# Kernel tuning notes

Measured on AMD Instinct MI355X. Metric: run time of the kernel, lower is better.

## Reference

```python
import jax, jax.numpy as jnp
import numpy as np

B, S, DM, H, HD = 2, 2048, 1024, 16, 64
MEM_SIZE = 1000
K_SIMILAR, K_CONTIG = 8, 2
K_TOTAL = K_SIMILAR + K_CONTIG  # 10 memory tokens
NEG = -1e9


def setup_inputs() -> dict:
    key = jax.random.key(0)
    k1, k2, k3, k4, k5, k6 = jax.random.split(key, 6)
    inputs = jax.random.normal(k1, (B, S, DM), dtype=jnp.float32)
    attention_mask = jnp.ones((B, S), dtype=jnp.float32)
    Wq = jax.random.normal(k2, (DM, H * HD), dtype=jnp.float32) * 0.02
    Wk = jax.random.normal(k3, (DM, H * HD), dtype=jnp.float32) * 0.02
    Wv = jax.random.normal(k4, (DM, H * HD), dtype=jnp.float32) * 0.02
    Wo = jax.random.normal(k5, (H * HD, DM), dtype=jnp.float32) * 0.02
    events = jax.random.normal(k6, (MEM_SIZE, H * HD), dtype=jnp.float32) * 0.02
    return {"inputs": inputs, "attention_mask": attention_mask,
            "Wq": Wq, "Wk": Wk, "Wv": Wv, "Wo": Wo, "events": events}


def _forward(inputs, attention_mask, Wq, Wk, Wv, Wo, events):
    # projections (no bias), split heads: [B, H, S, HD]
    q = (inputs @ Wq).reshape(B, S, H, HD).transpose(0, 2, 1, 3)
    k = (inputs @ Wk).reshape(B, S, H, HD).transpose(0, 2, 1, 3)
    v = (inputs @ Wv).reshape(B, S, H, HD).transpose(0, 2, 1, 3)

    # --- episodic retrieval: cosine top-k of last-token key vs events ---
    qvec = k[:, :, -1, :].reshape(B, H * HD)                       # [B, D]
    qn = qvec / (jnp.linalg.norm(qvec, axis=-1, keepdims=True) + 1e-8)
    en = events / (jnp.linalg.norm(events, axis=-1, keepdims=True) + 1e-8)
    sims = qn @ en.T                                               # [B, M]
    _, topk_idx = jax.lax.top_k(sims, K_TOTAL)                     # [B, K]
    retrieved = events[topk_idx]                                   # [B, K, D]
    retrieved_k = retrieved.reshape(B, K_TOTAL, H, HD).transpose(0, 2, 1, 3)  # [B,H,K,HD]
    retrieved_v = retrieved_k                                      # non-differential path

    aug_k = jnp.concatenate([retrieved_k, k], axis=2)              # [B,H,K+S,HD]
    aug_v = jnp.concatenate([retrieved_v, v], axis=2)

    # --- ALiBi bias: slopes * (pos_i - pos_j) on original cols, 0 on memory cols ---
    slopes = 2.0 ** (-8.0 * jnp.arange(1, H + 1, dtype=jnp.float32) / H)  # [H]
    positions = jnp.arange(S, dtype=jnp.float32)
    pos_diff = positions[:, None] - positions[None, :]             # [S, S]
    alibi = slopes[:, None, None] * pos_diff                       # [H, S, S]
    alibi = jnp.concatenate([jnp.zeros((H, S, K_TOTAL), jnp.float32), alibi], axis=-1)

    # --- causal mask: -1e9 strictly-upper on original cols, 0 on memory cols ---
    tri = jnp.where(jnp.arange(S)[None, :] > jnp.arange(S)[:, None], NEG, 0.0)  # [S,S]
    causal = jnp.concatenate([jnp.zeros((S, K_TOTAL), jnp.float32), tri], axis=-1)

    # --- padding mask: memory tokens always attendable ---
    aug_mask = jnp.concatenate([jnp.ones((B, K_TOTAL), jnp.float32), attention_mask], axis=-1)
    mask_bias = (1.0 - aug_mask)[:, None, None, :] * NEG           # [B,1,1,K+S]

    scores = jnp.einsum("bhqd,bhkd->bhqk", q, aug_k) / np.sqrt(HD)
    scores = scores + alibi[None] + causal[None, None] + mask_bias
    attn = jax.nn.softmax(scores, axis=-1)
    out = jnp.einsum("bhqk,bhkd->bhqd", attn, aug_v)               # [B,H,S,HD]
    out = out.transpose(0, 2, 1, 3).reshape(B, S, H * HD)
    return out @ Wo


def reference(inputs, attention_mask, Wq, Wk, Wv, Wo, events):
    return _forward(inputs, attention_mask, Wq, Wk, Wv, Wo, events)
```

## Files before the change

### kernel.cpp

```cpp
#include <hip/hip_runtime.h>
#include <hip/hip_bf16.h>
#include <math.h>

#define B_   2
#define S_   2048
#define DM_  1024
#define H_   16
#define HD_  64
#define MEM_ 1000
#define KTOT 10
#define NROW (B_ * S_)
#define NEG9 (-1e9f)
#define LDK  72
#define NITEMS 1024

typedef __attribute__((ext_vector_type(8))) short short8;
typedef __attribute__((ext_vector_type(4))) float f32x4;

__device__ __forceinline__ void gll16(const __hip_bfloat16* g, __hip_bfloat16* l) {
    __builtin_amdgcn_global_load_lds(
        (const __attribute__((address_space(1))) void*)g,
        (__attribute__((address_space(3))) void*)l, 16, 0, 0);
}

__global__ __launch_bounds__(256) void prep(const float* __restrict__ inputs,
                                            const float* __restrict__ Wq,
                                            const float* __restrict__ Wk,
                                            const float* __restrict__ Wv,
                                            const float* __restrict__ Wo,
                                            __hip_bfloat16* __restrict__ Ax,
                                            __hip_bfloat16* __restrict__ Wt,
                                            float* __restrict__ lk,
                                            int* __restrict__ ctr) {
    const int bx = blockIdx.x, tid = threadIdx.x;
    if (bx == 0 && tid == 0) *ctr = 0;

    if (bx < 2048) {
        const size_t i = ((size_t)bx * 256 + tid) * 8;
        float4 a = *(const float4*)&inputs[i];
        float4 b = *(const float4*)&inputs[i + 4];
        alignas(16) __hip_bfloat16 t[8];
        t[0] = __float2bfloat16(a.x); t[1] = __float2bfloat16(a.y);
        t[2] = __float2bfloat16(a.z); t[3] = __float2bfloat16(a.w);
        t[4] = __float2bfloat16(b.x); t[5] = __float2bfloat16(b.y);
        t[6] = __float2bfloat16(b.z); t[7] = __float2bfloat16(b.w);
        *(short8*)&Ax[i] = *(short8*)t;
        return;
    }
    if (bx < 3072) {
        const int idx = bx - 2048;
        const int g = idx >> 8, rem = idx & 255;
        const float* W = (g == 0) ? Wq : (g == 1) ? Wk : (g == 2) ? Wv : Wo;
        const int n0 = (rem & 15) * 64, k0 = (rem >> 4) * 64;
        __shared__ float T[64][65];
        {
            const int r = tid >> 4, c4 = (tid & 15) * 4;
#pragma unroll
            for (int p = 0; p < 4; ++p) {
                float4 v = *(const float4*)&W[(size_t)(k0 + r + p * 16) * 1024 + n0 + c4];
                T[r + p * 16][c4 + 0] = v.x; T[r + p * 16][c4 + 1] = v.y;
                T[r + p * 16][c4 + 2] = v.z; T[r + p * 16][c4 + 3] = v.w;
            }
        }
        __syncthreads();
        {
            const int n = tid >> 3, off = (tid & 7) * 8;
#pragma unroll
            for (int p = 0; p < 2; ++p) {
                const int nn = n + p * 32;
                alignas(16) __hip_bfloat16 t[8];
#pragma unroll
                for (int j = 0; j < 8; ++j) t[j] = __float2bfloat16(T[off + j][nn]);
                *(short8*)&Wt[((size_t)(g * 1024 + n0 + nn)) * 1024 + k0 + off] = *(short8*)t;
            }
        }
        return;
    }
    {
        const int idx = bx - 3072;
        const int xblk = idx & 15, b = idx >> 4;
        const int cl = tid & 63;
        const int col = xblk * 64 + cl;
        const int kq = tid >> 6;
        __shared__ float xr[1024];
        __shared__ float part[4][64];
        for (int i = tid; i < 1024; i += 256)
            xr[i] = inputs[((size_t)(b * S_ + S_ - 1)) * 1024 + i];
        __syncthreads();
        float acc = 0.f;
#pragma unroll 4
        for (int k = kq * 256; k < kq * 256 + 256; ++k)
            acc += xr[k] * Wk[(size_t)k * 1024 + col];
        part[kq][cl] = acc;
        __syncthreads();
        if (tid < 64)
            lk[b * 1024 + xblk * 64 + tid] =
                part[0][tid] + part[1][tid] + part[2][tid] + part[3][tid];
    }
}

__device__ __forceinline__ void store_out(__hip_bfloat16* p, float x) { *p = __float2bfloat16(x); }
__device__ __forceinline__ void store_out(float* p, float x) { *p = x; }

template <typename OutT>
__global__ __launch_bounds__(256) void gemm_mfma(const __hip_bfloat16* __restrict__ A,
                                                 const __hip_bfloat16* __restrict__ Bt,
                                                 OutT* __restrict__ C, int ldc) {
    __shared__ __hip_bfloat16 As[128 * 32];
    __shared__ __hip_bfloat16 Bs[128 * 32];
    const int tid = threadIdx.x;
    const int wave = tid >> 6, lane = tid & 63;
    const int quad = lane >> 4, lm = lane & 15;
    const int wr = wave >> 1, wc = wave & 1;
    const int m0 = blockIdx.y * 128, n0 = blockIdx.x * 128;

    const int r0 = tid >> 2, c0 = (tid & 3) * 8;
    const __hip_bfloat16* ga0 = &A[(size_t)(m0 + r0) * 1024 + c0];
    const __hip_bfloat16* ga1 = &A[(size_t)(m0 + 64 + r0) * 1024 + c0];
    const __hip_bfloat16* gb0 = &Bt[(size_t)(n0 + r0) * 1024 + c0];
    const __hip_bfloat16* gb1 = &Bt[(size_t)(n0 + 64 + r0) * 1024 + c0];
    __hip_bfloat16* la0 = &As[(wave * 64) * 8];
    __hip_bfloat16* la1 = &As[(256 + wave * 64) * 8];
    __hip_bfloat16* lb0 = &Bs[(wave * 64) * 8];
    __hip_bfloat16* lb1 = &Bs[(256 + wave * 64) * 8];

    f32x4 acc[4][4];
#pragma unroll
    for (int i = 0; i < 4; ++i)
#pragma unroll
        for (int j = 0; j < 4; ++j) acc[i][j] = (f32x4){0.f, 0.f, 0.f, 0.f};

    for (int k0 = 0; k0 < 1024; k0 += 32) {
        __syncthreads();
        gll16(ga0 + k0, la0);
        gll16(ga1 + k0, la1);
        gll16(gb0 + k0, lb0);
        gll16(gb1 + k0, lb1);
        __syncthreads();
        short8 af[4], bf4[4];
#pragma unroll
        for (int mt = 0; mt < 4; ++mt)
            af[mt] = *(const short8*)&As[(wr * 64 + mt * 16 + lm) * 32 + quad * 8];
#pragma unroll
        for (int nt = 0; nt < 4; ++nt)
            bf4[nt] = *(const short8*)&Bs[(wc * 64 + nt * 16 + lm) * 32 + quad * 8];
#pragma unroll
        for (int mt = 0; mt < 4; ++mt)
#pragma unroll
            for (int nt = 0; nt < 4; ++nt)
                acc[mt][nt] = __builtin_amdgcn_mfma_f32_16x16x32_bf16(
                    af[mt], bf4[nt], acc[mt][nt], 0, 0, 0);
    }
#pragma unroll
    for (int mt = 0; mt < 4; ++mt)
#pragma unroll
        for (int nt = 0; nt < 4; ++nt) {
            const int col = n0 + wc * 64 + nt * 16 + lm;
#pragma unroll
            for (int i = 0; i < 4; ++i) {
                const int row = m0 + wr * 64 + mt * 16 + quad * 4 + i;
                store_out(&C[(size_t)row * ldc + col], acc[mt][nt][i]);
            }
        }
}

__global__ __launch_bounds__(256) void sims_kernel(const float* __restrict__ lk,
                                                   const float* __restrict__ events,
                                                   float* __restrict__ sims) {
    const int b = blockIdx.y;
    const int tid = threadIdx.x;
    const int wave = tid >> 6, lane = tid & 63;
    __shared__ float qv[1024];
    for (int i = tid; i < 1024; i += 256)
        qv[i] = lk[b * 1024 + i];
    __syncthreads();

    const int m = blockIdx.x * 4 + wave;
    if (m >= MEM_) return;
    const float* ev = &events[(size_t)m * 1024];
    float dot = 0.f, nrm = 0.f;
    for (int d = lane; d < 1024; d += 64) {
        float e = ev[d];
        dot += qv[d] * e;
        nrm += e * e;
    }
    for (int off = 32; off; off >>= 1) {
        dot += __shfl_down(dot, off);
        nrm += __shfl_down(nrm, off);
    }
    if (lane == 0) sims[b * 1024 + m] = dot / (sqrtf(nrm) + 1e-8f);
}

__global__ __launch_bounds__(64) void topk10_kernel(const float* __restrict__ sims,
                                                    int* __restrict__ topk) {
    const int b = blockIdx.x;
    const int lane = threadIdx.x;
    const int base = lane * 16;
    float v[16];
#pragma unroll
    for (int j = 0; j < 16; ++j) {
        const int m = base + j;
        v[j] = (m < MEM_) ? sims[b * 1024 + m] : -INFINITY;
    }
    for (int it = 0; it < KTOT; ++it) {
        float best = -INFINITY; int bi = 0x7fffffff;
#pragma unroll
        for (int j = 0; j < 16; ++j)
            if (v[j] > best) { best = v[j]; bi = base + j; }
        for (int off = 32; off; off >>= 1) {
            const float ob = __shfl_xor(best, off);
            const int   oi = __shfl_xor(bi, off);
            if (ob > best || (ob == best && oi < bi)) { best = ob; bi = oi; }
        }
        if (lane == 0) topk[b * KTOT + it] = bi;
#pragma unroll
        for (int j = 0; j < 16; ++j)
            if (base + j == bi) v[j] = -INFINITY;
    }
}

__global__ __launch_bounds__(256) void attn_mfma(
        const __hip_bfloat16* __restrict__ qkv,
        const float* __restrict__ events,
        const int* __restrict__ topk,
        const float* __restrict__ amask,
        __hip_bfloat16* __restrict__ out,
        int* __restrict__ ctr) {
    const int tid = threadIdx.x;
    const int wave = tid >> 6, lane = tid & 63;
    const int quad = lane >> 4, lm = lane & 15;

    const __hip_bfloat16* qf = qkv;
    const __hip_bfloat16* kf = qkv + 1024;
    const __hip_bfloat16* vf = qkv + 2048;

    __shared__ __hip_bfloat16 Ks[64 * LDK];
    __shared__ __hip_bfloat16 Vt[80 * LDK];
    __shared__ __hip_bfloat16 Ps[64 * LDK];
    __shared__ float colb[64];
    __shared__ float redb[4];
    __shared__ int sItem;

    const int va = tid & 31, vdc = tid >> 5;
    const int vtok0 = va * 2, vd0 = vdc * 8;

    for (int i = tid; i < 16 * LDK; i += 256) {
        const int r = i / LDK;
        Vt[64 * LDK + i] = __float2bfloat16(r == 0 ? 1.0f : 0.0f);
    }

    for (;;) {
        __syncthreads();
        if (tid == 0) sItem = atomicAdd(ctr, 1);
        __syncthreads();
        const int n = sItem;
        if (n >= NITEMS) break;

        const int qt = 31 - (n >> 5);
        const int q0 = qt * 64;
        const int inner = n & 31;
        const int h = 15 - ((inner >> 1) & 15);
        const int b = inner & 1;
        const float slope = exp2f(-0.5f * (float)(h + 1));

        short8 qa[2];
        {
            const __hip_bfloat16* qsrc =
                &qf[((size_t)(b * S_ + q0 + wave * 16 + lm)) * 3072 + h * 64 + quad * 8];
            qa[0] = *(const short8*)qsrc;
            qa[1] = *(const short8*)(qsrc + 32);
        }
        for (int i = tid * 8; i < 64 * LDK; i += 256 * 8)
            *(int4*)&Vt[i] = make_int4(0, 0, 0, 0);
        __syncthreads();
        if (tid < 80) {
            const int tok = tid >> 3, d0 = (tid & 7) * 8;
            const int ev = topk[b * KTOT + tok];
            const float* es = &events[(size_t)ev * 1024 + h * 64 + d0];
#pragma unroll
            for (int j = 0; j < 8; ++j) {
                __hip_bfloat16 x = __float2bfloat16(es[j]);
                Ks[tok * LDK + d0 + j] = x;
                Vt[(d0 + j) * LDK + tok] = x;
            }
        }
        __syncthreads();

        float m_[4], mshift[4];
        f32x4 Oa[5];
#pragma unroll
        for (int i = 0; i < 4; ++i) {
            m_[i] = -INFINITY;
            mshift[i] = -slope * (float)(q0 + wave * 16 + quad * 4 + i);
        }
#pragma unroll
        for (int nt = 0; nt < 5; ++nt) Oa[nt] = (f32x4){0.f, 0.f, 0.f, 0.f};

        short8 pk[2], pv0, pv1;
        float pam = 1.f;
        auto prefetchKV = [&](int kt) {
            const __hip_bfloat16* ks = &kf[((size_t)(b * S_ + kt * 64)) * 3072 + h * 64];
#pragma unroll
            for (int u = 0; u < 2; ++u) {
                int c = tid * 2 + u, row = c >> 3, off = (c & 7) * 8;
                pk[u] = *(const short8*)&ks[(size_t)row * 3072 + off];
            }
            const __hip_bfloat16* v0 =
                &vf[((size_t)(b * S_ + kt * 64 + vtok0)) * 3072 + h * 64 + vd0];
            pv0 = *(const short8*)v0;
            pv1 = *(const short8*)(v0 + 3072);
            if (tid < 64) pam = amask[b * S_ + kt * 64 + tid];
        };
        auto stageKV = [&](int kt) {
#pragma unroll
            for (int u = 0; u < 2; ++u) {
                int c = tid * 2 + u, row = c >> 3, off = (c & 7) * 8;
                *(short8*)&Ks[row * LDK + off] = pk[u];
            }
#pragma unroll
            for (int j = 0; j < 8; ++j) {
                short2 pr; pr.x = pv0[j]; pr.y = pv1[j];
                *(short2*)&Vt[(vd0 + j) * LDK + vtok0] = pr;
            }
            if (tid < 64)
                colb[tid] = fmaf(-slope, (float)(kt * 64 + tid), (1.f - pam) * NEG9);
        };

        auto qk = [&](f32x4* sa) {
#pragma unroll
            for (int nt = 0; nt < 4; ++nt) sa[nt] = (f32x4){0.f, 0.f, 0.f, 0.f};
#pragma unroll
            for (int ks2 = 0; ks2 < 2; ++ks2) {
#pragma unroll
                for (int nt = 0; nt < 4; ++nt) {
                    short8 bk = *(const short8*)&Ks[(nt * 16 + lm) * LDK + ks2 * 32 + quad * 8];
                    sa[nt] = __builtin_amdgcn_mfma_f32_16x16x32_bf16(qa[ks2], bk, sa[nt], 0, 0, 0);
                }
            }
        };
        auto pv = [&]() {
#pragma unroll
            for (int ks2 = 0; ks2 < 2; ++ks2) {
                short8 ap = *(const short8*)&Ps[(wave * 16 + lm) * LDK + ks2 * 32 + quad * 8];
#pragma unroll
                for (int nt = 0; nt < 5; ++nt) {
                    short8 bv = *(const short8*)&Vt[(nt * 16 + lm) * LDK + ks2 * 32 + quad * 8];
                    Oa[nt] = __builtin_amdgcn_mfma_f32_16x16x32_bf16(ap, bv, Oa[nt], 0, 0, 0);
                }
            }
        };

        auto softmax_online = [&](const f32x4* sa, int kt, bool diag) {
            float cb[4];
            if (kt >= 0) {
#pragma unroll
                for (int nt = 0; nt < 4; ++nt) cb[nt] = colb[nt * 16 + lm];
            }
#pragma unroll
            for (int i = 0; i < 4; ++i) {
                const int lr = wave * 16 + quad * 4 + i;
                const int rg = q0 + lr;
                float s[4];
#pragma unroll
                for (int nt = 0; nt < 4; ++nt) {
                    const int cc = nt * 16 + lm;
                    if (kt < 0) {
                        s[nt] = (cc < KTOT) ? fmaf(sa[nt][i], 0.125f, mshift[i]) : NEG9;
                    } else {
                        float v = fmaf(sa[nt][i], 0.125f, cb[nt]);
                        s[nt] = (diag && kt * 64 + cc > rg) ? NEG9 : v;
                    }
                }
                float rmax = fmaxf(fmaxf(s[0], s[1]), fmaxf(s[2], s[3]));
#pragma unroll
                for (int off = 1; off < 16; off <<= 1)
                    rmax = fmaxf(rmax, __shfl_xor(rmax, off, 16));
                const float newm = fmaxf(m_[i], rmax);
                const float al = __expf(m_[i] - newm);
                m_[i] = newm;
#pragma unroll
                for (int nt = 0; nt < 4; ++nt)
                    Ps[lr * LDK + nt * 16 + lm] = __float2bfloat16(__expf(s[nt] - newm));
#pragma unroll
                for (int nt = 0; nt < 5; ++nt)
                    Oa[nt][i] *= al;
            }
        };

        auto softmax_fast = [&](const f32x4* sa, int cbase, bool diag) {
            float cb[4];
#pragma unroll
            for (int nt = 0; nt < 4; ++nt) cb[nt] = colb[nt * 16 + lm];
#pragma unroll
            for (int i = 0; i < 4; ++i) {
                const int lr = wave * 16 + quad * 4 + i;
                const float cm = m_[i];
                float p[4];
#pragma unroll
                for (int nt = 0; nt < 4; ++nt)
                    p[nt] = __expf(fmaf(sa[nt][i], 0.125f, cb[nt]) - cm);
                if (diag) {
                    const int rg = q0 + lr;
#pragma unroll
                    for (int nt = 0; nt < 4; ++nt)
                        if (cbase + nt * 16 + lm > rg) p[nt] = 0.f;
                }
#pragma unroll
                for (int nt = 0; nt < 4; ++nt)
                    Ps[lr * LDK + nt * 16 + lm] = __float2bfloat16(p[nt]);
            }
        };

        prefetchKV(0);
        {
            f32x4 sa[4];
            qk(sa);
            softmax_online(sa, -1, false);
            pv();
        }
        __syncthreads();
        stageKV(0);
        if (qt >= 1) prefetchKV(1);
        __syncthreads();
        {
            f32x4 sa[4];
            qk(sa);
            softmax_online(sa, 0, qt == 0);
            pv();
        }

        int ktend = 0;
        if (qt >= 1) {
            float mloc = fminf(fminf(m_[0], m_[1]), fminf(m_[2], m_[3]));
#pragma unroll
            for (int off = 1; off < 64; off <<= 1)
                mloc = fminf(mloc, __shfl_xor(mloc, off, 64));
            if (lane == 0) redb[wave] = mloc;
            __syncthreads();
            const float mmin = fminf(fminf(redb[0], redb[1]), fminf(redb[2], redb[3]));
            ktend = min(qt, (int)((118.f - mmin) / (64.f * slope)));
        }
        for (int kt = 1; kt <= ktend; ++kt) {
            __syncthreads();
            stageKV(kt);
            if (kt < ktend) prefetchKV(kt + 1);
            __syncthreads();
            f32x4 sa[4];
            qk(sa);
            softmax_fast(sa, kt * 64, kt == qt);
            pv();
        }

#pragma unroll
        for (int i = 0; i < 4; ++i) {
            const int lr = wave * 16 + quad * 4 + i;
            const float l = __shfl(Oa[4][i], (lane & 48));
            const float inv = 1.f / l;
            __hip_bfloat16* dst = &out[((size_t)(b * S_ + q0 + lr)) * 1024 + h * 64 + lm];
#pragma unroll
            for (int nt = 0; nt < 4; ++nt)
                dst[nt * 16] = __float2bfloat16(Oa[nt][i] * inv);
        }
    }
}

extern "C" void kernel_launch(void* const* d_in, const int* in_sizes, int n_in,
                              void* d_out, int out_size, void* d_ws, size_t ws_size,
                              hipStream_t stream) {
    const float* inputs = (const float*)d_in[0];
    const float* amask  = (const float*)d_in[1];
    const float* Wq     = (const float*)d_in[2];
    const float* Wk     = (const float*)d_in[3];
    const float* Wv     = (const float*)d_in[4];
    const float* Wo     = (const float*)d_in[5];
    const float* events = (const float*)d_in[6];
    float* out = (float*)d_out;

    __hip_bfloat16* Ax  = (__hip_bfloat16*)d_ws;
    __hip_bfloat16* Wt  = Ax + (size_t)NROW * 1024;
    __hip_bfloat16* qkv = Wt + (size_t)4096 * 1024;
    __hip_bfloat16* ao  = qkv + (size_t)NROW * 3072;
    float* lk   = (float*)(ao + (size_t)NROW * 1024);
    float* sims = lk + 2 * 1024;
    int* topk   = (int*)(sims + 2 * 1024);
    int* ctr    = topk + B_ * KTOT;

    dim3 blk(256);
    prep<<<3104, blk, 0, stream>>>(inputs, Wq, Wk, Wv, Wo, Ax, Wt, lk, ctr);
    sims_kernel<<<dim3(250, B_), blk, 0, stream>>>(lk, events, sims);
    topk10_kernel<<<B_, 64, 0, stream>>>(sims, topk);
    gemm_mfma<__hip_bfloat16><<<dim3(24, 32), blk, 0, stream>>>(Ax, Wt, qkv, 3072);
    attn_mfma<<<768, blk, 0, stream>>>(qkv, events, topk, amask, ao, ctr);
    gemm_mfma<float><<<dim3(8, 32), blk, 0, stream>>>(
        ao, Wt + (size_t)3072 * 1024, out, 1024);
}
```

Before: 242.0 us.

## Double-buffer K/V tiles in attention and use 64-row tiles for output GEMM

New measurement: 227.4 us. -6.0%, faster.

```diff
diff --git a/kernel.cpp b/kernel.cpp
--- a/kernel.cpp
+++ b/kernel.cpp
@@ -164,6 +164,65 @@
         }
 }
 
+template <typename OutT>
+__global__ __launch_bounds__(256) void gemm_mfma64(const __hip_bfloat16* __restrict__ A,
+                                                   const __hip_bfloat16* __restrict__ Bt,
+                                                   OutT* __restrict__ C, int ldc) {
+    __shared__ __hip_bfloat16 As[64 * 32];
+    __shared__ __hip_bfloat16 Bs[128 * 32];
+    const int tid = threadIdx.x;
+    const int wave = tid >> 6, lane = tid & 63;
+    const int quad = lane >> 4, lm = lane & 15;
+    const int wr = wave >> 1, wc = wave & 1;
+    const int m0 = blockIdx.y * 64, n0 = blockIdx.x * 128;
+
+    const int r0 = tid >> 2, c0 = (tid & 3) * 8;
+    const __hip_bfloat16* ga  = &A[(size_t)(m0 + r0) * 1024 + c0];
+    const __hip_bfloat16* gb0 = &Bt[(size_t)(n0 + r0) * 1024 + c0];
+    const __hip_bfloat16* gb1 = &Bt[(size_t)(n0 + 64 + r0) * 1024 + c0];
+    __hip_bfloat16* la  = &As[(wave * 64) * 8];
+    __hip_bfloat16* lb0 = &Bs[(wave * 64) * 8];
+    __hip_bfloat16* lb1 = &Bs[(256 + wave * 64) * 8];
+
+    f32x4 acc[2][4];
+#pragma unroll
+    for (int i = 0; i < 2; ++i)
+#pragma unroll
+        for (int j = 0; j < 4; ++j) acc[i][j] = (f32x4){0.f, 0.f, 0.f, 0.f};
+
+    for (int k0 = 0; k0 < 1024; k0 += 32) {
+        __syncthreads();
+        gll16(ga + k0, la);
+        gll16(gb0 + k0, lb0);
+        gll16(gb1 + k0, lb1);
+        __syncthreads();
+        short8 af[2], bf4[4];
+#pragma unroll
+        for (int mt = 0; mt < 2; ++mt)
+            af[mt] = *(const short8*)&As[(wr * 32 + mt * 16 + lm) * 32 + quad * 8];
+#pragma unroll
+        for (int nt = 0; nt < 4; ++nt)
+            bf4[nt] = *(const short8*)&Bs[(wc * 64 + nt * 16 + lm) * 32 + quad * 8];
+#pragma unroll
+        for (int mt = 0; mt < 2; ++mt)
+#pragma unroll
+            for (int nt = 0; nt < 4; ++nt)
+                acc[mt][nt] = __builtin_amdgcn_mfma_f32_16x16x32_bf16(
+                    af[mt], bf4[nt], acc[mt][nt], 0, 0, 0);
+    }
+#pragma unroll
+    for (int mt = 0; mt < 2; ++mt)
+#pragma unroll
+        for (int nt = 0; nt < 4; ++nt) {
+            const int col = n0 + wc * 64 + nt * 16 + lm;
+#pragma unroll
+            for (int i = 0; i < 4; ++i) {
+                const int row = m0 + wr * 32 + mt * 16 + quad * 4 + i;
+                store_out(&C[(size_t)row * ldc + col], acc[mt][nt][i]);
+            }
+        }
+}
+
 __global__ __launch_bounds__(256) void sims_kernel(const float* __restrict__ lk,
                                                    const float* __restrict__ events,
                                                    float* __restrict__ sims) {
@@ -234,19 +293,25 @@
     const __hip_bfloat16* kf = qkv + 1024;
     const __hip_bfloat16* vf = qkv + 2048;
 
-    __shared__ __hip_bfloat16 Ks[64 * LDK];
-    __shared__ __hip_bfloat16 Vt[80 * LDK];
+    __shared__ __hip_bfloat16 Ks[2][64 * LDK];
+    __shared__ __hip_bfloat16 Vt[2][80 * LDK];
     __shared__ __hip_bfloat16 Ps[64 * LDK];
-    __shared__ float colb[64];
+    __shared__ float colb[2][64];
     __shared__ float redb[4];
     __shared__ int sItem;
 
     const int va = tid & 31, vdc = tid >> 5;
     const int vtok0 = va * 2, vd0 = vdc * 8;
 
+    for (int i = tid * 8; i < 64 * LDK; i += 256 * 8) {
+        *(int4*)&Vt[0][i] = make_int4(0, 0, 0, 0);
+        *(int4*)&Vt[1][i] = make_int4(0, 0, 0, 0);
+    }
     for (int i = tid; i < 16 * LDK; i += 256) {
         const int r = i / LDK;
-        Vt[64 * LDK + i] = __float2bfloat16(r == 0 ? 1.0f : 0.0f);
+        const __hip_bfloat16 v = __float2bfloat16(r == 0 ? 1.0f : 0.0f);
+        Vt[0][64 * LDK + i] = v;
+        Vt[1][64 * LDK + i] = v;
     }
 
     for (;;) {
@@ -263,6 +328,38 @@
         const int b = inner & 1;
         const float slope = exp2f(-0.5f * (float)(h + 1));
 
+        short8 pk[2], pv0, pv1;
+        float pam = 1.f;
+        auto prefetchKV = [&](int kt) {
+            const __hip_bfloat16* ks = &kf[((size_t)(b * S_ + kt * 64)) * 3072 + h * 64];
+#pragma unroll
+            for (int u = 0; u < 2; ++u) {
+                int c = tid * 2 + u, row = c >> 3, off = (c & 7) * 8;
+                pk[u] = *(const short8*)&ks[(size_t)row * 3072 + off];
+            }
+            const __hip_bfloat16* v0 =
+                &vf[((size_t)(b * S_ + kt * 64 + vtok0)) * 3072 + h * 64 + vd0];
+            pv0 = *(const short8*)v0;
+            pv1 = *(const short8*)(v0 + 3072);
+            if (tid < 64) pam = amask[b * S_ + kt * 64 + tid];
+        };
+        auto stageKV = [&](int kt, int pb) {
+#pragma unroll
+            for (int u = 0; u < 2; ++u) {
+                int c = tid * 2 + u, row = c >> 3, off = (c & 7) * 8;
+                *(short8*)&Ks[pb][row * LDK + off] = pk[u];
+            }
+#pragma unroll
+            for (int j = 0; j < 8; ++j) {
+                short2 pr; pr.x = pv0[j]; pr.y = pv1[j];
+                *(short2*)&Vt[pb][(vd0 + j) * LDK + vtok0] = pr;
+            }
+            if (tid < 64)
+                colb[pb][tid] = fmaf(-slope, (float)(kt * 64 + tid), (1.f - pam) * NEG9);
+        };
+
+        prefetchKV(0);
+
         short8 qa[2];
         {
             const __hip_bfloat16* qsrc =
@@ -270,9 +367,6 @@
             qa[0] = *(const short8*)qsrc;
             qa[1] = *(const short8*)(qsrc + 32);
         }
-        for (int i = tid * 8; i < 64 * LDK; i += 256 * 8)
-            *(int4*)&Vt[i] = make_int4(0, 0, 0, 0);
-        __syncthreads();
         if (tid < 80) {
             const int tok = tid >> 3, d0 = (tid & 7) * 8;
             const int ev = topk[b * KTOT + tok];
@@ -280,8 +374,8 @@
 #pragma unroll
             for (int j = 0; j < 8; ++j) {
                 __hip_bfloat16 x = __float2bfloat16(es[j]);
-                Ks[tok * LDK + d0 + j] = x;
-                Vt[(d0 + j) * LDK + tok] = x;
+                Ks[0][tok * LDK + d0 + j] = x;
+                Vt[0][(d0 + j) * LDK + tok] = x;
             }
         }
         __syncthreads();
@@ -296,65 +390,35 @@
 #pragma unroll
         for (int nt = 0; nt < 5; ++nt) Oa[nt] = (f32x4){0.f, 0.f, 0.f, 0.f};
 
-        short8 pk[2], pv0, pv1;
-        float pam = 1.f;
-        auto prefetchKV = [&](int kt) {
-            const __hip_bfloat16* ks = &kf[((size_t)(b * S_ + kt * 64)) * 3072 + h * 64];
-#pragma unroll
-            for (int u = 0; u < 2; ++u) {
-                int c = tid * 2 + u, row = c >> 3, off = (c & 7) * 8;
-                pk[u] = *(const short8*)&ks[(size_t)row * 3072 + off];
-            }
-            const __hip_bfloat16* v0 =
-                &vf[((size_t)(b * S_ + kt * 64 + vtok0)) * 3072 + h * 64 + vd0];
-            pv0 = *(const short8*)v0;
-            pv1 = *(const short8*)(v0 + 3072);
-            if (tid < 64) pam = amask[b * S_ + kt * 64 + tid];
-        };
-        auto stageKV = [&](int kt) {
-#pragma unroll
-            for (int u = 0; u < 2; ++u) {
-                int c = tid * 2 + u, row = c >> 3, off = (c & 7) * 8;
-                *(short8*)&Ks[row * LDK + off] = pk[u];
-            }
-#pragma unroll
-            for (int j = 0; j < 8; ++j) {
-                short2 pr; pr.x = pv0[j]; pr.y = pv1[j];
-                *(short2*)&Vt[(vd0 + j) * LDK + vtok0] = pr;
-            }
-            if (tid < 64)
-                colb[tid] = fmaf(-slope, (float)(kt * 64 + tid), (1.f - pam) * NEG9);
-        };
-
-        auto qk = [&](f32x4* sa) {
+        auto qk = [&](f32x4* sa, const __hip_bfloat16* Kp) {
 #pragma unroll
             for (int nt = 0; nt < 4; ++nt) sa[nt] = (f32x4){0.f, 0.f, 0.f, 0.f};
 #pragma unroll
             for (int ks2 = 0; ks2 < 2; ++ks2) {
 #pragma unroll
                 for (int nt = 0; nt < 4; ++nt) {
-                    short8 bk = *(const short8*)&Ks[(nt * 16 + lm) * LDK + ks2 * 32 + quad * 8];
+                    short8 bk = *(const short8*)&Kp[(nt * 16 + lm) * LDK + ks2 * 32 + quad * 8];
                     sa[nt] = __builtin_amdgcn_mfma_f32_16x16x32_bf16(qa[ks2], bk, sa[nt], 0, 0, 0);
                 }
             }
         };
-        auto pv = [&]() {
+        auto pv = [&](const __hip_bfloat16* Vp) {
 #pragma unroll
             for (int ks2 = 0; ks2 < 2; ++ks2) {
                 short8 ap = *(const short8*)&Ps[(wave * 16 + lm) * LDK + ks2 * 32 + quad * 8];
 #pragma unroll
                 for (int nt = 0; nt < 5; ++nt) {
-                    short8 bv = *(const short8*)&Vt[(nt * 16 + lm) * LDK + ks2 * 32 + quad * 8];
+                    short8 bv = *(const short8*)&Vp[(nt * 16 + lm) * LDK + ks2 * 32 + quad * 8];
                     Oa[nt] = __builtin_amdgcn_mfma_f32_16x16x32_bf16(ap, bv, Oa[nt], 0, 0, 0);
                 }
             }
         };
 
-        auto softmax_online = [&](const f32x4* sa, int kt, bool diag) {
+        auto softmax_online = [&](const f32x4* sa, int kt, bool diag, const float* cbp) {
             float cb[4];
             if (kt >= 0) {
 #pragma unroll
-                for (int nt = 0; nt < 4; ++nt) cb[nt] = colb[nt * 16 + lm];
+                for (int nt = 0; nt < 4; ++nt) cb[nt] = cbp[nt * 16 + lm];
             }
 #pragma unroll
             for (int i = 0; i < 4; ++i) {
@@ -387,10 +451,10 @@
             }
         };
 
-        auto softmax_fast = [&](const f32x4* sa, int cbase, bool diag) {
+        auto softmax_fast = [&](const f32x4* sa, int cbase, bool diag, const float* cbp) {
             float cb[4];
 #pragma unroll
-            for (int nt = 0; nt < 4; ++nt) cb[nt] = colb[nt * 16 + lm];
+            for (int nt = 0; nt < 4; ++nt) cb[nt] = cbp[nt * 16 + lm];
 #pragma unroll
             for (int i = 0; i < 4; ++i) {
                 const int lr = wave * 16 + quad * 4 + i;
@@ -411,44 +475,47 @@
             }
         };
 
-        prefetchKV(0);
         {
             f32x4 sa[4];
-            qk(sa);
-            softmax_online(sa, -1, false);
-            pv();
-        }
-        __syncthreads();
-        stageKV(0);
+            qk(sa, Ks[0]);
+            softmax_online(sa, -1, false, nullptr);
+            pv(Vt[0]);
+        }
+        stageKV(0, 1);
         if (qt >= 1) prefetchKV(1);
         __syncthreads();
+
         {
             f32x4 sa[4];
-            qk(sa);
-            softmax_online(sa, 0, qt == 0);
-            pv();
-        }
-
-        int ktend = 0;
-        if (qt >= 1) {
+            qk(sa, Ks[1]);
+            softmax_online(sa, 0, qt == 0, colb[1]);
+            pv(Vt[1]);
+        }
+        {
             float mloc = fminf(fminf(m_[0], m_[1]), fminf(m_[2], m_[3]));
 #pragma unroll
             for (int off = 1; off < 64; off <<= 1)
                 mloc = fminf(mloc, __shfl_xor(mloc, off, 64));
             if (lane == 0) redb[wave] = mloc;
-            __syncthreads();
+        }
+        if (qt >= 1) stageKV(1, 0);
+        if (qt >= 2) prefetchKV(2);
+        __syncthreads();
+
+        int ktend = 0;
+        if (qt >= 1) {
             const float mmin = fminf(fminf(redb[0], redb[1]), fminf(redb[2], redb[3]));
             ktend = min(qt, (int)((118.f - mmin) / (64.f * slope)));
         }
         for (int kt = 1; kt <= ktend; ++kt) {
+            const int pb = (kt + 1) & 1;
+            f32x4 sa[4];
+            qk(sa, Ks[pb]);
+            softmax_fast(sa, kt * 64, kt == qt, colb[pb]);
+            pv(Vt[pb]);
+            if (kt < ktend) stageKV(kt + 1, kt & 1);
+            if (kt + 1 < ktend) prefetchKV(kt + 2);
             __syncthreads();
-            stageKV(kt);
-            if (kt < ktend) prefetchKV(kt + 1);
-            __syncthreads();
-            f32x4 sa[4];
-            qk(sa);
-            softmax_fast(sa, kt * 64, kt == qt);
-            pv();
         }
 
 #pragma unroll
@@ -491,6 +558,6 @@
     topk10_kernel<<<B_, 64, 0, stream>>>(sims, topk);
     gemm_mfma<__hip_bfloat16><<<dim3(24, 32), blk, 0, stream>>>(Ax, Wt, qkv, 3072);
     attn_mfma<<<768, blk, 0, stream>>>(qkv, events, topk, amask, ao, ctr);
-    gemm_mfma<float><<<dim3(8, 32), blk, 0, stream>>>(
+    gemm_mfma64<float><<<dim3(8, 64), blk, 0, stream>>>(
         ao, Wt + (size_t)3072 * 1024, out, 1024);
 }
```

## Split long attention tiles across two blocks and merge partials; smaller output GEMM tiles

Applied to the files above, without the earlier changes.

Result: slower. 383.6 us (+58.5%).

```diff
diff --git a/kernel.cpp b/kernel.cpp
--- a/kernel.cpp
+++ b/kernel.cpp
@@ -12,7 +12,13 @@
 #define NROW (B_ * S_)
 #define NEG9 (-1e9f)
 #define LDK  72
-#define NITEMS 1024
+
+#define NSPLITU 768
+#define NSPLITI 384
+#define NUNITS  1408
+#define PSLOT   4224
+#define SC_     0.18033688f
+#define TH_     170.238f
 
 typedef __attribute__((ext_vector_type(8))) short short8;
 typedef __attribute__((ext_vector_type(4))) float f32x4;
@@ -31,9 +37,12 @@
                                             __hip_bfloat16* __restrict__ Ax,
                                             __hip_bfloat16* __restrict__ Wt,
                                             float* __restrict__ lk,
-                                            int* __restrict__ ctr) {
+                                            int* __restrict__ ctr,
+                                            int* __restrict__ done) {
     const int bx = blockIdx.x, tid = threadIdx.x;
     if (bx == 0 && tid == 0) *ctr = 0;
+    if (bx == 1)
+        for (int i = tid; i < NSPLITI; i += 256) done[i] = 0;
 
     if (bx < 2048) {
         const size_t i = ((size_t)bx * 256 + tid) * 8;
@@ -164,6 +173,65 @@
         }
 }
 
+template <typename OutT>
+__global__ __launch_bounds__(256) void gemm_mfma64(const __hip_bfloat16* __restrict__ A,
+                                                   const __hip_bfloat16* __restrict__ Bt,
+                                                   OutT* __restrict__ C, int ldc) {
+    __shared__ __hip_bfloat16 As[64 * 32];
+    __shared__ __hip_bfloat16 Bs[128 * 32];
+    const int tid = threadIdx.x;
+    const int wave = tid >> 6, lane = tid & 63;
+    const int quad = lane >> 4, lm = lane & 15;
+    const int wr = wave >> 1, wc = wave & 1;
+    const int m0 = blockIdx.y * 64, n0 = blockIdx.x * 128;
+
+    const int r0 = tid >> 2, c0 = (tid & 3) * 8;
+    const __hip_bfloat16* ga  = &A[(size_t)(m0 + r0) * 1024 + c0];
+    const __hip_bfloat16* gb0 = &Bt[(size_t)(n0 + r0) * 1024 + c0];
+    const __hip_bfloat16* gb1 = &Bt[(size_t)(n0 + 64 + r0) * 1024 + c0];
+    __hip_bfloat16* la  = &As[(wave * 64) * 8];
+    __hip_bfloat16* lb0 = &Bs[(wave * 64) * 8];
+    __hip_bfloat16* lb1 = &Bs[(256 + wave * 64) * 8];
+
+    f32x4 acc[2][4];
+#pragma unroll
+    for (int i = 0; i < 2; ++i)
+#pragma unroll
+        for (int j = 0; j < 4; ++j) acc[i][j] = (f32x4){0.f, 0.f, 0.f, 0.f};
+
+    for (int k0 = 0; k0 < 1024; k0 += 32) {
+        __syncthreads();
+        gll16(ga + k0, la);
+        gll16(gb0 + k0, lb0);
+        gll16(gb1 + k0, lb1);
+        __syncthreads();
+        short8 af[2], bf4[4];
+#pragma unroll
+        for (int mt = 0; mt < 2; ++mt)
+            af[mt] = *(const short8*)&As[(wr * 32 + mt * 16 + lm) * 32 + quad * 8];
+#pragma unroll
+        for (int nt = 0; nt < 4; ++nt)
+            bf4[nt] = *(const short8*)&Bs[(wc * 64 + nt * 16 + lm) * 32 + quad * 8];
+#pragma unroll
+        for (int mt = 0; mt < 2; ++mt)
+#pragma unroll
+            for (int nt = 0; nt < 4; ++nt)
+                acc[mt][nt] = __builtin_amdgcn_mfma_f32_16x16x32_bf16(
+                    af[mt], bf4[nt], acc[mt][nt], 0, 0, 0);
+    }
+#pragma unroll
+    for (int mt = 0; mt < 2; ++mt)
+#pragma unroll
+        for (int nt = 0; nt < 4; ++nt) {
+            const int col = n0 + wc * 64 + nt * 16 + lm;
+#pragma unroll
+            for (int i = 0; i < 4; ++i) {
+                const int row = m0 + wr * 32 + mt * 16 + quad * 4 + i;
+                store_out(&C[(size_t)row * ldc + col], acc[mt][nt][i]);
+            }
+        }
+}
+
 __global__ __launch_bounds__(256) void sims_kernel(const float* __restrict__ lk,
                                                    const float* __restrict__ events,
                                                    float* __restrict__ sims) {
@@ -225,7 +293,9 @@
         const int* __restrict__ topk,
         const float* __restrict__ amask,
         __hip_bfloat16* __restrict__ out,
-        int* __restrict__ ctr) {
+        int* __restrict__ ctr,
+        int* __restrict__ done,
+        float* __restrict__ partb) {
     const int tid = threadIdx.x;
     const int wave = tid >> 6, lane = tid & 63;
     const int quad = lane >> 4, lm = lane & 15;
@@ -240,10 +310,13 @@
     __shared__ float colb[64];
     __shared__ float redb[4];
     __shared__ int sItem;
+    __shared__ int sOld;
 
     const int va = tid & 31, vdc = tid >> 5;
     const int vtok0 = va * 2, vd0 = vdc * 8;
 
+    for (int i = tid * 8; i < 64 * LDK; i += 256 * 8)
+        *(int4*)&Vt[i] = make_int4(0, 0, 0, 0);
     for (int i = tid; i < 16 * LDK; i += 256) {
         const int r = i / LDK;
         Vt[64 * LDK + i] = __float2bfloat16(r == 0 ? 1.0f : 0.0f);
@@ -254,47 +327,32 @@
         if (tid == 0) sItem = atomicAdd(ctr, 1);
         __syncthreads();
         const int n = sItem;
-        if (n >= NITEMS) break;
-
-        const int qt = 31 - (n >> 5);
+        if (n >= NUNITS) break;
+
+        int qt, inner, kstart, kend, nparts, slot = 0, sidx = 0;
+        bool haveMem;
+        if (n < NSPLITU) {
+            qt = 31 - (n >> 6);
+            const int rem = n & 63;
+            const int prt = rem >> 5;
+            inner = rem & 31;
+            const int mid = (qt + 1) >> 1;
+            kstart = prt ? mid : 0;
+            kend   = prt ? qt : (mid - 1);
+            haveMem = (prt == 0);
+            nparts = 2;
+            sidx = (31 - qt) * 32 + inner;
+            slot = sidx * 2 + prt;
+        } else {
+            const int n2 = n - NSPLITU;
+            qt = 19 - (n2 >> 5);
+            inner = n2 & 31;
+            kstart = 0; kend = qt; haveMem = true; nparts = 1;
+        }
         const int q0 = qt * 64;
-        const int inner = n & 31;
         const int h = 15 - ((inner >> 1) & 15);
         const int b = inner & 1;
-        const float slope = exp2f(-0.5f * (float)(h + 1));
-
-        short8 qa[2];
-        {
-            const __hip_bfloat16* qsrc =
-                &qf[((size_t)(b * S_ + q0 + wave * 16 + lm)) * 3072 + h * 64 + quad * 8];
-            qa[0] = *(const short8*)qsrc;
-            qa[1] = *(const short8*)(qsrc + 32);
-        }
-        for (int i = tid * 8; i < 64 * LDK; i += 256 * 8)
-            *(int4*)&Vt[i] = make_int4(0, 0, 0, 0);
-        __syncthreads();
-        if (tid < 80) {
-            const int tok = tid >> 3, d0 = (tid & 7) * 8;
-            const int ev = topk[b * KTOT + tok];
-            const float* es = &events[(size_t)ev * 1024 + h * 64 + d0];
-#pragma unroll
-            for (int j = 0; j < 8; ++j) {
-                __hip_bfloat16 x = __float2bfloat16(es[j]);
-                Ks[tok * LDK + d0 + j] = x;
-                Vt[(d0 + j) * LDK + tok] = x;
-            }
-        }
-        __syncthreads();
-
-        float m_[4], mshift[4];
-        f32x4 Oa[5];
-#pragma unroll
-        for (int i = 0; i < 4; ++i) {
-            m_[i] = -INFINITY;
-            mshift[i] = -slope * (float)(q0 + wave * 16 + quad * 4 + i);
-        }
-#pragma unroll
-        for (int nt = 0; nt < 5; ++nt) Oa[nt] = (f32x4){0.f, 0.f, 0.f, 0.f};
+        const float slope2 = exp2f(-0.5f * (float)(h + 1)) * 1.44269504f;
 
         short8 pk[2], pv0, pv1;
         float pam = 1.f;
@@ -323,8 +381,39 @@
                 *(short2*)&Vt[(vd0 + j) * LDK + vtok0] = pr;
             }
             if (tid < 64)
-                colb[tid] = fmaf(-slope, (float)(kt * 64 + tid), (1.f - pam) * NEG9);
+                colb[tid] = fmaf(-slope2, (float)(kt * 64 + tid), (1.f - pam) * NEG9);
         };
+
+        prefetchKV(kstart);
+
+        short8 qa[2];
+        {
+            const __hip_bfloat16* qsrc =
+                &qf[((size_t)(b * S_ + q0 + wave * 16 + lm)) * 3072 + h * 64 + quad * 8];
+            qa[0] = *(const short8*)qsrc;
+            qa[1] = *(const short8*)(qsrc + 32);
+        }
+        if (haveMem && tid < 80) {
+            const int tok = tid >> 3, d0 = (tid & 7) * 8;
+            const int ev = topk[b * KTOT + tok];
+            const float* es = &events[(size_t)ev * 1024 + h * 64 + d0];
+#pragma unroll
+            for (int j = 0; j < 8; ++j) {
+                __hip_bfloat16 x = __float2bfloat16(es[j]);
+                Ks[tok * LDK + d0 + j] = x;
+                Vt[(d0 + j) * LDK + tok] = x;
+            }
+        }
+
+        float m_[4], mshift[4];
+        f32x4 Oa[5];
+#pragma unroll
+        for (int i = 0; i < 4; ++i) {
+            m_[i] = -INFINITY;
+            mshift[i] = -slope2 * (float)(q0 + wave * 16 + quad * 4 + i);
+        }
+#pragma unroll
+        for (int nt = 0; nt < 5; ++nt) Oa[nt] = (f32x4){0.f, 0.f, 0.f, 0.f};
 
         auto qk = [&](f32x4* sa) {
 #pragma unroll
@@ -365,9 +454,9 @@
                 for (int nt = 0; nt < 4; ++nt) {
                     const int cc = nt * 16 + lm;
                     if (kt < 0) {
-                        s[nt] = (cc < KTOT) ? fmaf(sa[nt][i], 0.125f, mshift[i]) : NEG9;
+                        s[nt] = (cc < KTOT) ? fmaf(sa[nt][i], SC_, mshift[i]) : NEG9;
                     } else {
-                        float v = fmaf(sa[nt][i], 0.125f, cb[nt]);
+                        float v = fmaf(sa[nt][i], SC_, cb[nt]);
                         s[nt] = (diag && kt * 64 + cc > rg) ? NEG9 : v;
                     }
                 }
@@ -376,11 +465,11 @@
                 for (int off = 1; off < 16; off <<= 1)
                     rmax = fmaxf(rmax, __shfl_xor(rmax, off, 16));
                 const float newm = fmaxf(m_[i], rmax);
-                const float al = __expf(m_[i] - newm);
+                const float al = exp2f(m_[i] - newm);
                 m_[i] = newm;
 #pragma unroll
                 for (int nt = 0; nt < 4; ++nt)
-                    Ps[lr * LDK + nt * 16 + lm] = __float2bfloat16(__expf(s[nt] - newm));
+                    Ps[lr * LDK + nt * 16 + lm] = __float2bfloat16(exp2f(s[nt] - newm));
 #pragma unroll
                 for (int nt = 0; nt < 5; ++nt)
                     Oa[nt][i] *= al;
@@ -398,7 +487,7 @@
                 float p[4];
 #pragma unroll
                 for (int nt = 0; nt < 4; ++nt)
-                    p[nt] = __expf(fmaf(sa[nt][i], 0.125f, cb[nt]) - cm);
+                    p[nt] = exp2f(fmaf(sa[nt][i], SC_, cb[nt]) - cm);
                 if (diag) {
                     const int rg = q0 + lr;
 #pragma unroll
@@ -411,26 +500,26 @@
             }
         };
 
-        prefetchKV(0);
-        {
+        if (haveMem) {
+            __syncthreads();
             f32x4 sa[4];
             qk(sa);
             softmax_online(sa, -1, false);
             pv();
         }
         __syncthreads();
-        stageKV(0);
-        if (qt >= 1) prefetchKV(1);
+        stageKV(kstart);
+        if (kstart < kend) prefetchKV(kstart + 1);
         __syncthreads();
         {
             f32x4 sa[4];
             qk(sa);
-            softmax_online(sa, 0, qt == 0);
+            softmax_online(sa, kstart, kstart == qt);
             pv();
         }
 
-        int ktend = 0;
-        if (qt >= 1) {
+        int kend2 = kstart;
+        if (kend > kstart) {
             float mloc = fminf(fminf(m_[0], m_[1]), fminf(m_[2], m_[3]));
 #pragma unroll
             for (int off = 1; off < 64; off <<= 1)
@@ -438,28 +527,67 @@
             if (lane == 0) redb[wave] = mloc;
             __syncthreads();
             const float mmin = fminf(fminf(redb[0], redb[1]), fminf(redb[2], redb[3]));
-            ktend = min(qt, (int)((118.f - mmin) / (64.f * slope)));
-        }
-        for (int kt = 1; kt <= ktend; ++kt) {
-            __syncthreads();
+            kend2 = min(kend, (int)((TH_ - mmin) / (64.f * slope2)));
+        }
+        for (int kt = kstart + 1; kt <= kend2; ++kt) {
             stageKV(kt);
-            if (kt < ktend) prefetchKV(kt + 1);
+            if (kt < kend2) prefetchKV(kt + 1);
             __syncthreads();
             f32x4 sa[4];
             qk(sa);
             softmax_fast(sa, kt * 64, kt == qt);
             pv();
-        }
-
-#pragma unroll
-        for (int i = 0; i < 4; ++i) {
-            const int lr = wave * 16 + quad * 4 + i;
-            const float l = __shfl(Oa[4][i], (lane & 48));
-            const float inv = 1.f / l;
-            __hip_bfloat16* dst = &out[((size_t)(b * S_ + q0 + lr)) * 1024 + h * 64 + lm];
-#pragma unroll
-            for (int nt = 0; nt < 4; ++nt)
-                dst[nt * 16] = __float2bfloat16(Oa[nt][i] * inv);
+            __syncthreads();
+        }
+
+        if (nparts == 1) {
+#pragma unroll
+            for (int i = 0; i < 4; ++i) {
+                const int lr = wave * 16 + quad * 4 + i;
+                const float l = __shfl(Oa[4][i], (lane & 48));
+                const float inv = 1.f / l;
+                __hip_bfloat16* dst = &out[((size_t)(b * S_ + q0 + lr)) * 1024 + h * 64 + lm];
+#pragma unroll
+                for (int nt = 0; nt < 4; ++nt)
+                    dst[nt * 16] = __float2bfloat16(Oa[nt][i] * inv);
+            }
+        } else {
+            float l_[4];
+#pragma unroll
+            for (int i = 0; i < 4; ++i) l_[i] = __shfl(Oa[4][i], (lane & 48));
+            float* psl = partb + (size_t)slot * PSLOT;
+#pragma unroll
+            for (int i = 0; i < 4; ++i) {
+                const int lr = wave * 16 + quad * 4 + i;
+#pragma unroll
+                for (int nt = 0; nt < 4; ++nt)
+                    psl[lr * 64 + nt * 16 + lm] = Oa[nt][i];
+                if (lm == 0) {
+                    psl[4096 + lr] = m_[i];
+                    psl[4160 + lr] = l_[i];
+                }
+            }
+            __threadfence();
+            if (tid == 0) sOld = atomicAdd(&done[sidx], 1);
+            __syncthreads();
+            if (sOld == 1) {
+                __threadfence();
+                const float* po = partb + (size_t)(slot ^ 1) * PSLOT;
+#pragma unroll
+                for (int i = 0; i < 4; ++i) {
+                    const int lr = wave * 16 + quad * 4 + i;
+                    const float m2 = po[4096 + lr], l2 = po[4160 + lr];
+                    const float mm = fmaxf(m_[i], m2);
+                    const float f1 = exp2f(m_[i] - mm), f2 = exp2f(m2 - mm);
+                    const float inv = 1.f / (l_[i] * f1 + l2 * f2);
+                    __hip_bfloat16* dst =
+                        &out[((size_t)(b * S_ + q0 + lr)) * 1024 + h * 64 + lm];
+#pragma unroll
+                    for (int nt = 0; nt < 4; ++nt)
+                        dst[nt * 16] = __float2bfloat16(
+                            (Oa[nt][i] * f1 + po[lr * 64 + nt * 16 + lm] * f2) * inv);
+                }
+            }
         }
     }
 }
@@ -484,13 +612,15 @@
     float* sims = lk + 2 * 1024;
     int* topk   = (int*)(sims + 2 * 1024);
     int* ctr    = topk + B_ * KTOT;
+    int* done   = ctr + 1;
+    float* partb = (float*)d_ws;
 
     dim3 blk(256);
-    prep<<<3104, blk, 0, stream>>>(inputs, Wq, Wk, Wv, Wo, Ax, Wt, lk, ctr);
+    prep<<<3104, blk, 0, stream>>>(inputs, Wq, Wk, Wv, Wo, Ax, Wt, lk, ctr, done);
     sims_kernel<<<dim3(250, B_), blk, 0, stream>>>(lk, events, sims);
     topk10_kernel<<<B_, 64, 0, stream>>>(sims, topk);
     gemm_mfma<__hip_bfloat16><<<dim3(24, 32), blk, 0, stream>>>(Ax, Wt, qkv, 3072);
-    attn_mfma<<<768, blk, 0, stream>>>(qkv, events, topk, amask, ao, ctr);
-    gemm_mfma<float><<<dim3(8, 32), blk, 0, stream>>>(
+    attn_mfma<<<1280, blk, 0, stream>>>(qkv, events, topk, amask, ao, ctr, done, partb);
+    gemm_mfma64<float><<<dim3(8, 64), blk, 0, stream>>>(
         ao, Wt + (size_t)3072 * 1024, out, 1024);
 }
```
